# Optimization experiments

Measured on AMD Instinct MI355X. Metric: run time of the kernel, lower is better.

## Reference

```python
import jax, jax.numpy as jnp
import numpy as np

B, C_ENT, C_REL = 32768, 1000, 500


def setup_inputs() -> dict:
    key = jax.random.key(0)
    ks = jax.random.split(key, 6)
    return {
        "sub_input": jax.random.normal(ks[0], (B, C_ENT), dtype=jnp.float32),
        "relation_input": jax.random.normal(ks[1], (B, C_REL), dtype=jnp.float32),
        "obj_input": jax.random.normal(ks[2], (B, C_ENT), dtype=jnp.float32),
        "sub_target": jax.random.randint(ks[3], (B,), 0, C_ENT, dtype=jnp.int32),
        "relation_target": jax.random.randint(ks[4], (B,), 0, C_REL, dtype=jnp.int32),
        "obj_target": jax.random.randint(ks[5], (B,), 0, C_ENT, dtype=jnp.int32),
    }


def reference(sub_input, relation_input, obj_input, sub_target, relation_target, obj_target):
    s = jax.nn.softmax(sub_input, axis=1)
    r = jax.nn.softmax(relation_input, axis=1)
    o = jax.nn.softmax(obj_input, axis=1)
    b = s.shape[0]
    rows = jnp.arange(b)

    # ground-truth triplet probability
    gt = s[rows, sub_target] * r[rows, relation_target] * o[rows, obj_target]

    # top-2 values/indices per row (replaces full torch.sort)
    sv, si = jax.lax.top_k(s, 2)
    rv, ri = jax.lax.top_k(r, 2)
    ov, oi = jax.lax.top_k(o, 2)

    # all three argmaxes match the targets?
    cond = (si[:, 0] == sub_target) & (ri[:, 0] == relation_target) & (oi[:, 0] == obj_target)

    # 8 combinations of top-2 probs; second-smallest of the 8 (torch.sort ascending, index 1)
    tmp = (sv[:, :, None, None] * rv[:, None, :, None] * ov[:, None, None, :]).reshape(b, 8)
    second_smallest = jnp.sort(tmp, axis=1)[:, 1]

    top1 = sv[:, 0] * rv[:, 0] * ov[:, 0]
    pre = jnp.where(cond, second_smallest, top1)

    out = 1.0 - gt + pre
    return jnp.mean(jnp.maximum(out, 0.0))
```

## Files before the change

kernel.cpp:

```cpp
#include <hip/hip_runtime.h>
#include <float.h>
#include <limits.h>


constexpr int B     = 32768;
constexpr int C_ENT = 1000;
constexpr int C_REL = 500;
constexpr int NU    = 163840;
constexpr int UPW   = 16;
constexpr float LOG2E = 1.4426950408889634f;

__device__ inline float fast_exp2(float x) { return exp2f(x); }

__device__ inline const float4* unit_ptr(int u, const float* s, const float* r,
                                         const float* o) {
  const float* p;
  if (u < 2 * B)        p = s + ((size_t)(u >> 1) * C_ENT + (size_t)(u & 1) * C_REL);
  else if (u < 4 * B) { int v = u - 2 * B;
                        p = o + ((size_t)(v >> 1) * C_ENT + (size_t)(v & 1) * C_REL); }
  else                  p = r + (size_t)(u - 4 * B) * C_REL;
  return (const float4*)p;
}
__device__ inline int unit_ioff(int u) { return (u < 4 * B) ? (u & 1) * C_REL : 0; }

__device__ inline void unit_load(const float4* p4, int lane, float4& va, float4& vb) {
  va = make_float4(-FLT_MAX, -FLT_MAX, -FLT_MAX, -FLT_MAX);
  vb = va;
  if (lane <= 62) va = p4[2 * lane];
  if (lane <= 61) vb = p4[2 * lane + 1];
}

__device__ inline float4 unit_compute(const float4 va, const float4 vb,
                                      int lane, int ioff) {
  float m = fmaxf(fmaxf(fmaxf(va.x, va.y), fmaxf(va.z, va.w)),
                  fmaxf(fmaxf(vb.x, vb.y), fmaxf(vb.z, vb.w)));
#pragma unroll
  for (int off = 32; off; off >>= 1) m = fmaxf(m, __shfl_xor(m, off));
  const float m1 = m;
  const float nm1l = -m1 * LOG2E;

  float z = (fast_exp2(fmaf(va.x, LOG2E, nm1l)) + fast_exp2(fmaf(va.y, LOG2E, nm1l))) +
            (fast_exp2(fmaf(va.z, LOG2E, nm1l)) + fast_exp2(fmaf(va.w, LOG2E, nm1l))) +
            (fast_exp2(fmaf(vb.x, LOG2E, nm1l)) + fast_exp2(fmaf(vb.y, LOG2E, nm1l))) +
            (fast_exp2(fmaf(vb.z, LOG2E, nm1l)) + fast_exp2(fmaf(vb.w, LOG2E, nm1l)));

  const bool e0 = (va.x == m1), e1 = (va.y == m1), e2 = (va.z == m1), e3 = (va.w == m1);
  const bool e4 = (vb.x == m1), e5 = (vb.y == m1), e6 = (vb.z == m1), e7 = (vb.w == m1);
  const int cnt = ((int)e0 + (int)e1 + (int)e2 + (int)e3) +
                  ((int)e4 + (int)e5 + (int)e6 + (int)e7);
  float m2 = fmaxf(fmaxf(fmaxf(e0 ? -FLT_MAX : va.x, e1 ? -FLT_MAX : va.y),
                         fmaxf(e2 ? -FLT_MAX : va.z, e3 ? -FLT_MAX : va.w)),
                   fmaxf(fmaxf(e4 ? -FLT_MAX : vb.x, e5 ? -FLT_MAX : vb.y),
                         fmaxf(e6 ? -FLT_MAX : vb.z, e7 ? -FLT_MAX : vb.w)));
  const int li = e0 ? 0 : e1 ? 1 : e2 ? 2 : e3 ? 3 : e4 ? 4 : e5 ? 5 : e6 ? 6 : 7;

  const unsigned long long b1 = __ballot(cnt >= 1);
  const unsigned long long b2 = __ballot(cnt >= 2);
  const bool dup = (__popcll(b1) >= 2) || (b2 != 0ULL);
  const int src = __ffsll(b1) - 1;
  const int gidx = ioff + 8 * src + __shfl(li, src);

#pragma unroll
  for (int off = 32; off; off >>= 1) {
    z += __shfl_xor(z, off);
    m2 = fmaxf(m2, __shfl_xor(m2, off));
  }
  if (dup) m2 = m1;

  return make_float4(m1, m2, z, __int_as_float(gidx));
}

__global__ __launch_bounds__(256, 4) void stats_kernel(
    const float* __restrict__ s, const float* __restrict__ r, const float* __restrict__ o,
    float4* __restrict__ out4) {
  const int lane = threadIdx.x & 63;
  const int u0 = (blockIdx.x * 4 + (threadIdx.x >> 6)) * UPW;

  float4 Aa, Ab, Ba, Bb, Ca, Cb, Da, Db;
  unit_load(unit_ptr(u0 + 0, s, r, o), lane, Aa, Ab);
  unit_load(unit_ptr(u0 + 1, s, r, o), lane, Ba, Bb);
  unit_load(unit_ptr(u0 + 2, s, r, o), lane, Ca, Cb);

#pragma unroll
  for (int j = 0; j < UPW; j += 4) {
    float4 res;
    if (j + 3 < UPW) unit_load(unit_ptr(u0 + j + 3, s, r, o), lane, Da, Db);
    res = unit_compute(Aa, Ab, lane, unit_ioff(u0 + j + 0));
    if (lane == 0) out4[u0 + j + 0] = res;
    if (j + 4 < UPW) unit_load(unit_ptr(u0 + j + 4, s, r, o), lane, Aa, Ab);
    res = unit_compute(Ba, Bb, lane, unit_ioff(u0 + j + 1));
    if (lane == 0) out4[u0 + j + 1] = res;
    if (j + 5 < UPW) unit_load(unit_ptr(u0 + j + 5, s, r, o), lane, Ba, Bb);
    res = unit_compute(Ca, Cb, lane, unit_ioff(u0 + j + 2));
    if (lane == 0) out4[u0 + j + 2] = res;
    if (j + 6 < UPW) unit_load(unit_ptr(u0 + j + 6, s, r, o), lane, Ca, Cb);
    res = unit_compute(Da, Db, lane, unit_ioff(u0 + j + 3));
    if (lane == 0) out4[u0 + j + 3] = res;
  }
}

__device__ inline void merge_halves(float4 a, float4 b,
                                    float& m1, float& m2, float& Z, int& idx) {
  m1 = fmaxf(a.x, b.x);
  Z  = a.z * fast_exp2((a.x - m1) * LOG2E) + b.z * fast_exp2((b.x - m1) * LOG2E);
  m2 = fmaxf(fminf(a.x, b.x), (a.x >= b.x) ? a.y : b.y);
  idx = (b.x > a.x) ? __float_as_int(b.w) : __float_as_int(a.w);
}

__global__ __launch_bounds__(256) void combine_kernel(
    const float4* __restrict__ st4,
    const float* __restrict__ s, const float* __restrict__ r, const float* __restrict__ o,
    const int* __restrict__ st, const int* __restrict__ rt, const int* __restrict__ ot,
    float* __restrict__ out) {
  const int row = blockIdx.x * 256 + threadIdx.x;

  const float4 sa = st4[2 * row],         sb = st4[2 * row + 1];
  const float4 oa = st4[2 * B + 2 * row], ob = st4[2 * B + 2 * row + 1];
  const float4 rr = st4[4 * B + row];
  const int ts = st[row], tr = rt[row], to = ot[row];
  const float xs = s[(size_t)row * C_ENT + ts];
  const float xr = r[(size_t)row * C_REL + tr];
  const float xo = o[(size_t)row * C_ENT + to];

  float sm1, sm2, sZ; int si;
  float om1, om2, oZ; int oi;
  merge_halves(sa, sb, sm1, sm2, sZ, si);
  merge_halves(oa, ob, om1, om2, oZ, oi);
  const float rm1 = rr.x, rm2 = rr.y, rZ = rr.z;
  const int ri = __float_as_int(rr.w);

  const float sI = 1.0f / sZ, rI = 1.0f / rZ, oI = 1.0f / oZ;
  const float sp1 = fast_exp2((sm2 - sm1) * LOG2E) * sI;
  const float rp1 = fast_exp2((rm2 - rm1) * LOG2E) * rI;
  const float op1 = fast_exp2((om2 - om1) * LOG2E) * oI;
  const float spt = fast_exp2((xs - sm1) * LOG2E) * sI;
  const float rpt = fast_exp2((xr - rm1) * LOG2E) * rI;
  const float opt = fast_exp2((xo - om1) * LOG2E) * oI;

  const float gt   = spt * rpt * opt;
  const float top1 = sI * rI * oI;
  const float c1 = sI  * rp1 * op1;
  const float c2 = sp1 * rI  * op1;
  const float c3 = sp1 * rp1 * oI;
  const float second = fminf(c1, fminf(c2, c3));
  const bool cond = (si == ts) && (ri == tr) && (oi == to);
  const float pre = cond ? second : top1;
  float val = fmaxf(1.0f - gt + pre, 0.0f) * (1.0f / (float)B);

#pragma unroll
  for (int off = 32; off; off >>= 1) val += __shfl_xor(val, off);
  __shared__ float lds[4];
  if ((threadIdx.x & 63) == 0) lds[threadIdx.x >> 6] = val;
  __syncthreads();
  if (threadIdx.x == 0)
    atomicAdd(out, (lds[0] + lds[1]) + (lds[2] + lds[3]));
}


__device__ inline void combine_stats(float& m1, int& i1, float& m2, float& Z,
                                     float bm1, int bi1, float bm2, float bZ) {
  bool bwin = (bm1 > m1) || (bm1 == m1 && bi1 < i1);
  float wm1 = bwin ? bm1 : m1;
  int   wi1 = bwin ? bi1 : i1;
  float wm2 = bwin ? bm2 : m2;
  float lm1 = bwin ? m1  : bm1;
  float wZ  = bwin ? bZ  : Z;
  float lZ  = bwin ? Z   : bZ;
  m1 = wm1; i1 = wi1;
  m2 = fmaxf(wm2, lm1);
  Z  = wZ + lZ * __expf(lm1 - wm1);
}

template<int NK, int C4>
__device__ inline void row_stats(const float* __restrict__ row, int lane, int target,
                                 float& p_top1, float& p_top2, int& amax, float& p_tgt) {
  const float4* row4 = (const float4*)row;
  float4 v[NK];
#pragma unroll
  for (int k = 0; k < NK; ++k) {
    int idx = lane + 64 * k;
    v[k] = (idx < C4) ? row4[idx] : make_float4(-FLT_MAX, -FLT_MAX, -FLT_MAX, -FLT_MAX);
  }
  float m1 = -FLT_MAX, m2 = -FLT_MAX;
  int   i1 = 0x7fffffff;
#pragma unroll
  for (int k = 0; k < NK; ++k) {
    int base = 4 * (lane + 64 * k);
    float a0 = v[k].x, a1 = v[k].y, a2 = v[k].z, a3 = v[k].w;
    if (a0 > m1) { m2 = m1; m1 = a0; i1 = base;     } else if (a0 > m2) m2 = a0;
    if (a1 > m1) { m2 = m1; m1 = a1; i1 = base + 1; } else if (a1 > m2) m2 = a1;
    if (a2 > m1) { m2 = m1; m1 = a2; i1 = base + 2; } else if (a2 > m2) m2 = a2;
    if (a3 > m1) { m2 = m1; m1 = a3; i1 = base + 3; } else if (a3 > m2) m2 = a3;
  }
  float Z = 0.f;
#pragma unroll
  for (int k = 0; k < NK; ++k) {
    Z += __expf(v[k].x - m1); Z += __expf(v[k].y - m1);
    Z += __expf(v[k].z - m1); Z += __expf(v[k].w - m1);
  }
#pragma unroll
  for (int off = 32; off > 0; off >>= 1) {
    float bm1 = __shfl_xor(m1, off);
    int   bi1 = __shfl_xor(i1, off);
    float bm2 = __shfl_xor(m2, off);
    float bZ  = __shfl_xor(Z,  off);
    combine_stats(m1, i1, m2, Z, bm1, bi1, bm2, bZ);
  }
  float invZ = 1.0f / Z;
  float xt   = row[target];
  p_top1 = invZ;
  p_top2 = __expf(m2 - m1) * invZ;
  p_tgt  = __expf(xt - m1) * invZ;
  amax   = i1;
}

__global__ __launch_bounds__(256) void rank_loss_atomic_kernel(
    const float* __restrict__ s, const float* __restrict__ r, const float* __restrict__ o,
    const int* __restrict__ st, const int* __restrict__ rt, const int* __restrict__ ot,
    float* __restrict__ out) {
  const int wid  = threadIdx.x >> 6;
  const int lane = threadIdx.x & 63;
  const int row  = blockIdx.x * 4 + wid;

  const int tS = st[row], tR = rt[row], tO = ot[row];
  float sp0, sp1, spt; int sa;
  float rp0, rp1, rpt; int ra;
  float op0, op1, opt; int oa;
  row_stats<4, C_ENT / 4>(s + (size_t)row * C_ENT, lane, tS, sp0, sp1, sa, spt);
  row_stats<2, C_REL / 4>(r + (size_t)row * C_REL, lane, tR, rp0, rp1, ra, rpt);
  row_stats<4, C_ENT / 4>(o + (size_t)row * C_ENT, lane, tO, op0, op1, oa, opt);

  if (lane == 0) {
    float gt   = spt * rpt * opt;
    float top1 = sp0 * rp0 * op0;
    float c1 = sp0 * rp1 * op1;
    float c2 = sp1 * rp0 * op1;
    float c3 = sp1 * rp1 * op0;
    float second = fminf(c1, fminf(c2, c3));
    bool cond = (sa == tS) && (ra == tR) && (oa == tO);
    float pre = cond ? second : top1;
    atomicAdd(out, fmaxf(1.0f - gt + pre, 0.0f) * (1.0f / (float)B));
  }
}

extern "C" void kernel_launch(void* const* d_in, const int* in_sizes, int n_in,
                              void* d_out, int out_size, void* d_ws, size_t ws_size,
                              hipStream_t stream) {
  const float* s  = (const float*)d_in[0];
  const float* r  = (const float*)d_in[1];
  const float* o  = (const float*)d_in[2];
  const int*   st = (const int*)d_in[3];
  const int*   rt = (const int*)d_in[4];
  const int*   ot = (const int*)d_in[5];
  float* out = (float*)d_out;

  hipMemsetAsync(d_out, 0, sizeof(float), stream);
  if (ws_size >= (size_t)NU * sizeof(float4)) {
    float4* stat4 = (float4*)d_ws;
    stats_kernel<<<NU / UPW / 4, 256, 0, stream>>>(s, r, o, stat4);
    combine_kernel<<<B / 256, 256, 0, stream>>>(stat4, s, r, o, st, rt, ot, out);
  } else {
    rank_loss_atomic_kernel<<<B / 4, 256, 0, stream>>>(s, r, o, st, rt, ot, out);
  }
}
```

Before: 336.0 us.

## Restructure stats kernel to one thread per row with LDS-staged transposed tiles

Replaces the wave-per-half-row softmax statistics kernel with a 64-thread block that handles 64 rows, staging coalesced float4 loads through double-buffered LDS tiles so each thread streams its own row. Max, second max, argmax and the sum of exponentials are kept as online per-thread statistics, with no cross-lane shuffles. The target logit is captured during the pass, so the combine kernel no longer does scattered gathers into the big input matrices. The cost is LDS traffic, heavier per-thread register use and only 2560 single-wave blocks. The argmax tie handling also changes from the previous duplicate-detection logic.

New measurement: 824.0 us. +145.2%, slower.

```diff
diff --git a/kernel.cpp b/kernel.cpp
--- a/kernel.cpp
+++ b/kernel.cpp
@@ -1,126 +1,154 @@
 #include <hip/hip_runtime.h>
 #include <float.h>
-#include <limits.h>
 
 
 constexpr int B     = 32768;
 constexpr int C_ENT = 1000;
 constexpr int C_REL = 500;
-constexpr int NU    = 163840;
-constexpr int UPW   = 16;
 constexpr float LOG2E = 1.4426950408889634f;
 
-__device__ inline float fast_exp2(float x) { return exp2f(x); }
-
-__device__ inline const float4* unit_ptr(int u, const float* s, const float* r,
-                                         const float* o) {
-  const float* p;
-  if (u < 2 * B)        p = s + ((size_t)(u >> 1) * C_ENT + (size_t)(u & 1) * C_REL);
-  else if (u < 4 * B) { int v = u - 2 * B;
-                        p = o + ((size_t)(v >> 1) * C_ENT + (size_t)(v & 1) * C_REL); }
-  else                  p = r + (size_t)(u - 4 * B) * C_REL;
-  return (const float4*)p;
-}
-__device__ inline int unit_ioff(int u) { return (u < 4 * B) ? (u & 1) * C_REL : 0; }
-
-__device__ inline void unit_load(const float4* p4, int lane, float4& va, float4& vb) {
-  va = make_float4(-FLT_MAX, -FLT_MAX, -FLT_MAX, -FLT_MAX);
-  vb = va;
-  if (lane <= 62) va = p4[2 * lane];
-  if (lane <= 61) vb = p4[2 * lane + 1];
-}
-
-__device__ inline float4 unit_compute(const float4 va, const float4 vb,
-                                      int lane, int ioff) {
-  float m = fmaxf(fmaxf(fmaxf(va.x, va.y), fmaxf(va.z, va.w)),
-                  fmaxf(fmaxf(vb.x, vb.y), fmaxf(vb.z, vb.w)));
-#pragma unroll
-  for (int off = 32; off; off >>= 1) m = fmaxf(m, __shfl_xor(m, off));
-  const float m1 = m;
-  const float nm1l = -m1 * LOG2E;
-
-  float z = (fast_exp2(fmaf(va.x, LOG2E, nm1l)) + fast_exp2(fmaf(va.y, LOG2E, nm1l))) +
-            (fast_exp2(fmaf(va.z, LOG2E, nm1l)) + fast_exp2(fmaf(va.w, LOG2E, nm1l))) +
-            (fast_exp2(fmaf(vb.x, LOG2E, nm1l)) + fast_exp2(fmaf(vb.y, LOG2E, nm1l))) +
-            (fast_exp2(fmaf(vb.z, LOG2E, nm1l)) + fast_exp2(fmaf(vb.w, LOG2E, nm1l)));
-
-  const bool e0 = (va.x == m1), e1 = (va.y == m1), e2 = (va.z == m1), e3 = (va.w == m1);
-  const bool e4 = (vb.x == m1), e5 = (vb.y == m1), e6 = (vb.z == m1), e7 = (vb.w == m1);
-  const int cnt = ((int)e0 + (int)e1 + (int)e2 + (int)e3) +
-                  ((int)e4 + (int)e5 + (int)e6 + (int)e7);
-  float m2 = fmaxf(fmaxf(fmaxf(e0 ? -FLT_MAX : va.x, e1 ? -FLT_MAX : va.y),
-                         fmaxf(e2 ? -FLT_MAX : va.z, e3 ? -FLT_MAX : va.w)),
-                   fmaxf(fmaxf(e4 ? -FLT_MAX : vb.x, e5 ? -FLT_MAX : vb.y),
-                         fmaxf(e6 ? -FLT_MAX : vb.z, e7 ? -FLT_MAX : vb.w)));
-  const int li = e0 ? 0 : e1 ? 1 : e2 ? 2 : e3 ? 3 : e4 ? 4 : e5 ? 5 : e6 ? 6 : 7;
-
-  const unsigned long long b1 = __ballot(cnt >= 1);
-  const unsigned long long b2 = __ballot(cnt >= 2);
-  const bool dup = (__popcll(b1) >= 2) || (b2 != 0ULL);
-  const int src = __ffsll(b1) - 1;
-  const int gidx = ioff + 8 * src + __shfl(li, src);
-
-#pragma unroll
-  for (int off = 32; off; off >>= 1) {
-    z += __shfl_xor(z, off);
-    m2 = fmaxf(m2, __shfl_xor(m2, off));
-  }
-  if (dup) m2 = m1;
-
-  return make_float4(m1, m2, z, __int_as_float(gidx));
-}
-
-__global__ __launch_bounds__(256, 4) void stats_kernel(
+__device__ inline float fexp2(float x) { return exp2f(x); }
+
+
+__global__ __launch_bounds__(64, 4) void stats_kernel(
     const float* __restrict__ s, const float* __restrict__ r, const float* __restrict__ o,
-    float4* __restrict__ out4) {
-  const int lane = threadIdx.x & 63;
-  const int u0 = (blockIdx.x * 4 + (threadIdx.x >> 6)) * UPW;
-
-  float4 Aa, Ab, Ba, Bb, Ca, Cb, Da, Db;
-  unit_load(unit_ptr(u0 + 0, s, r, o), lane, Aa, Ab);
-  unit_load(unit_ptr(u0 + 1, s, r, o), lane, Ba, Bb);
-  unit_load(unit_ptr(u0 + 2, s, r, o), lane, Ca, Cb);
-
-#pragma unroll
-  for (int j = 0; j < UPW; j += 4) {
-    float4 res;
-    if (j + 3 < UPW) unit_load(unit_ptr(u0 + j + 3, s, r, o), lane, Da, Db);
-    res = unit_compute(Aa, Ab, lane, unit_ioff(u0 + j + 0));
-    if (lane == 0) out4[u0 + j + 0] = res;
-    if (j + 4 < UPW) unit_load(unit_ptr(u0 + j + 4, s, r, o), lane, Aa, Ab);
-    res = unit_compute(Ba, Bb, lane, unit_ioff(u0 + j + 1));
-    if (lane == 0) out4[u0 + j + 1] = res;
-    if (j + 5 < UPW) unit_load(unit_ptr(u0 + j + 5, s, r, o), lane, Ba, Bb);
-    res = unit_compute(Ca, Cb, lane, unit_ioff(u0 + j + 2));
-    if (lane == 0) out4[u0 + j + 2] = res;
-    if (j + 6 < UPW) unit_load(unit_ptr(u0 + j + 6, s, r, o), lane, Ca, Cb);
-    res = unit_compute(Da, Db, lane, unit_ioff(u0 + j + 3));
-    if (lane == 0) out4[u0 + j + 3] = res;
-  }
-}
+    const int* __restrict__ st, const int* __restrict__ rt, const int* __restrict__ ot,
+    float4* __restrict__ stat4, float* __restrict__ xtg) {
+  __shared__ float lds0[64 * 21];
+  __shared__ float lds1[64 * 21];
+  const int l = threadIdx.x;
+  const int u = blockIdx.x;
+  const int seg = u >> 9, rb = u & 511;
+
+  const float* mat; const int* tgt; int stride_f, coff_f;
+  if (seg < 2)      { mat = s; tgt = st; stride_f = C_ENT; coff_f = (seg & 1) * 500; }
+  else if (seg < 4) { mat = o; tgt = ot; stride_f = C_ENT; coff_f = (seg & 1) * 500; }
+  else              { mat = r; tgt = rt; stride_f = C_REL; coff_f = 0; }
+
+  const int row0 = rb * 64;
+  const float* segbase = mat + (size_t)row0 * stride_f + coff_f;
+
+  const float4* bp[5];
+  int wa[5];
+#pragma unroll
+  for (int j = 0; j < 5; ++j) {
+    const int f = j * 64 + l;
+    const int rl = f / 5, c = f - 5 * rl;
+    bp[j] = (const float4*)(segbase + (size_t)rl * stride_f) + c;
+    wa[j] = rl * 21 + c * 4;
+  }
+  const float* rp0 = &lds0[l * 21];
+  const float* rp1 = &lds1[l * 21];
+
+  const int t = tgt[row0 + l];
+  int d = t - coff_f;
+  float xt = 0.f;
+  float m1 = -FLT_MAX, m2 = -FLT_MAX, Z = 0.f;
+  int idx = 0, kb = 0;
+
+  auto compute = [&](const float* __restrict__ rowp) {
+    float a[20];
+#pragma unroll
+    for (int c = 0; c < 20; ++c) a[c] = rowp[c];
+    {
+      const unsigned du = (unsigned)d;
+      const float cand = rowp[du < 20u ? du : 19u];
+      if (du < 20u) xt = cand;
+      d -= 20;
+    }
+    const float b0 = fmaxf(fmaxf(a[0],  a[1]),  fmaxf(a[2],  a[3]));
+    const float b1 = fmaxf(fmaxf(a[4],  a[5]),  fmaxf(a[6],  a[7]));
+    const float b2 = fmaxf(fmaxf(a[8],  a[9]),  fmaxf(a[10], a[11]));
+    const float b3 = fmaxf(fmaxf(a[12], a[13]), fmaxf(a[14], a[15]));
+    const float b4 = fmaxf(fmaxf(a[16], a[17]), fmaxf(a[18], a[19]));
+    const float mc  = fmaxf(fmaxf(b0, b1), fmaxf(fmaxf(b2, b3), b4));
+    const float m1n = fmaxf(m1, mc);
+    const float nb  = -m1n * LOG2E;
+    float z0 = 0.f, z1 = 0.f, z2 = 0.f, z3 = 0.f;
+#pragma unroll
+    for (int c = 0; c < 20; c += 4) {
+      z0 += fexp2(fmaf(a[c],     LOG2E, nb));
+      z1 += fexp2(fmaf(a[c + 1], LOG2E, nb));
+      z2 += fexp2(fmaf(a[c + 2], LOG2E, nb));
+      z3 += fexp2(fmaf(a[c + 3], LOG2E, nb));
+    }
+    const float zc = (z0 + z1) + (z2 + z3);
+    Z = fmaf(Z, fexp2((m1 - m1n) * LOG2E), zc);
+    int lpos = 0;
+    const float m1b = m1;
+#pragma unroll
+    for (int c = 0; c < 20; ++c) {
+      const float av = a[c];
+      m2 = fmaxf(m2, fminf(m1, av));
+      const bool g = av > m1;
+      m1 = fmaxf(m1, av);
+      lpos = g ? c : lpos;
+    }
+    idx = (m1 > m1b) ? kb + lpos : idx;
+    kb += 20;
+  };
+  auto stage = [&](float* __restrict__ wb, const float4 v0, const float4 v1,
+                   const float4 v2, const float4 v3, const float4 v4) {
+    wb[wa[0]] = v0.x; wb[wa[0]+1] = v0.y; wb[wa[0]+2] = v0.z; wb[wa[0]+3] = v0.w;
+    wb[wa[1]] = v1.x; wb[wa[1]+1] = v1.y; wb[wa[1]+2] = v1.z; wb[wa[1]+3] = v1.w;
+    wb[wa[2]] = v2.x; wb[wa[2]+1] = v2.y; wb[wa[2]+2] = v2.z; wb[wa[2]+3] = v2.w;
+    wb[wa[3]] = v3.x; wb[wa[3]+1] = v3.y; wb[wa[3]+2] = v3.z; wb[wa[3]+3] = v3.w;
+    wb[wa[4]] = v4.x; wb[wa[4]+1] = v4.y; wb[wa[4]+2] = v4.z; wb[wa[4]+3] = v4.w;
+  };
+
+  float4 P0,P1,P2,P3,P4, Q0,Q1,Q2,Q3,Q4;
+  P0 = bp[0][0];  P1 = bp[1][0];  P2 = bp[2][0];  P3 = bp[3][0];  P4 = bp[4][0];
+  Q0 = bp[0][5];  Q1 = bp[1][5];  Q2 = bp[2][5];  Q3 = bp[3][5];  Q4 = bp[4][5];
+  stage(lds0, P0, P1, P2, P3, P4);
+  P0 = bp[0][10]; P1 = bp[1][10]; P2 = bp[2][10]; P3 = bp[3][10]; P4 = bp[4][10];
+  stage(lds1, Q0, Q1, Q2, Q3, Q4);
+  Q0 = bp[0][15]; Q1 = bp[1][15]; Q2 = bp[2][15]; Q3 = bp[3][15]; Q4 = bp[4][15];
+
+  for (int p = 0; p < 10; ++p) {
+    compute(rp0);
+    stage(lds0, P0, P1, P2, P3, P4);
+    P0 = bp[0][20]; P1 = bp[1][20]; P2 = bp[2][20]; P3 = bp[3][20]; P4 = bp[4][20];
+    compute(rp1);
+    stage(lds1, Q0, Q1, Q2, Q3, Q4);
+    Q0 = bp[0][25]; Q1 = bp[1][25]; Q2 = bp[2][25]; Q3 = bp[3][25]; Q4 = bp[4][25];
+    bp[0] += 10; bp[1] += 10; bp[2] += 10; bp[3] += 10; bp[4] += 10;
+  }
+  compute(rp0);
+  stage(lds0, P0, P1, P2, P3, P4);
+  P0 = bp[0][20]; P1 = bp[1][20]; P2 = bp[2][20]; P3 = bp[3][20]; P4 = bp[4][20];
+  compute(rp1);
+  stage(lds1, Q0, Q1, Q2, Q3, Q4);
+  compute(rp0);
+  stage(lds0, P0, P1, P2, P3, P4);
+  compute(rp1);
+  compute(rp0);
+
+  const int gr = seg * B + row0 + l;
+  stat4[gr] = make_float4(m1, m2, Z, __int_as_float(coff_f + idx));
+  xtg[gr] = xt;
+}
+
 
 __device__ inline void merge_halves(float4 a, float4 b,
                                     float& m1, float& m2, float& Z, int& idx) {
   m1 = fmaxf(a.x, b.x);
-  Z  = a.z * fast_exp2((a.x - m1) * LOG2E) + b.z * fast_exp2((b.x - m1) * LOG2E);
+  Z  = a.z * fexp2((a.x - m1) * LOG2E) + b.z * fexp2((b.x - m1) * LOG2E);
   m2 = fmaxf(fminf(a.x, b.x), (a.x >= b.x) ? a.y : b.y);
   idx = (b.x > a.x) ? __float_as_int(b.w) : __float_as_int(a.w);
 }
 
 __global__ __launch_bounds__(256) void combine_kernel(
-    const float4* __restrict__ st4,
-    const float* __restrict__ s, const float* __restrict__ r, const float* __restrict__ o,
+    const float4* __restrict__ st4, const float* __restrict__ xtg,
     const int* __restrict__ st, const int* __restrict__ rt, const int* __restrict__ ot,
     float* __restrict__ out) {
   const int row = blockIdx.x * 256 + threadIdx.x;
-
-  const float4 sa = st4[2 * row],         sb = st4[2 * row + 1];
-  const float4 oa = st4[2 * B + 2 * row], ob = st4[2 * B + 2 * row + 1];
+  const float4 sa = st4[row],         sb = st4[B + row];
+  const float4 oa = st4[2 * B + row], ob = st4[3 * B + row];
   const float4 rr = st4[4 * B + row];
   const int ts = st[row], tr = rt[row], to = ot[row];
-  const float xs = s[(size_t)row * C_ENT + ts];
-  const float xr = r[(size_t)row * C_REL + tr];
-  const float xo = o[(size_t)row * C_ENT + to];
+  const float xs = (ts < 500) ? xtg[row]           : xtg[B + row];
+  const float xo = (to < 500) ? xtg[2 * B + row]   : xtg[3 * B + row];
+  const float xr = xtg[4 * B + row];
 
   float sm1, sm2, sZ; int si;
   float om1, om2, oZ; int oi;
@@ -130,12 +158,12 @@
   const int ri = __float_as_int(rr.w);
 
   const float sI = 1.0f / sZ, rI = 1.0f / rZ, oI = 1.0f / oZ;
-  const float sp1 = fast_exp2((sm2 - sm1) * LOG2E) * sI;
-  const float rp1 = fast_exp2((rm2 - rm1) * LOG2E) * rI;
-  const float op1 = fast_exp2((om2 - om1) * LOG2E) * oI;
-  const float spt = fast_exp2((xs - sm1) * LOG2E) * sI;
-  const float rpt = fast_exp2((xr - rm1) * LOG2E) * rI;
-  const float opt = fast_exp2((xo - om1) * LOG2E) * oI;
+  const float sp1 = fexp2((sm2 - sm1) * LOG2E) * sI;
+  const float rp1 = fexp2((rm2 - rm1) * LOG2E) * rI;
+  const float op1 = fexp2((om2 - om1) * LOG2E) * oI;
+  const float spt = fexp2((xs - sm1) * LOG2E) * sI;
+  const float rpt = fexp2((xr - rm1) * LOG2E) * rI;
+  const float opt = fexp2((xo - om1) * LOG2E) * oI;
 
   const float gt   = spt * rpt * opt;
   const float top1 = sI * rI * oI;
@@ -149,11 +177,11 @@
 
 #pragma unroll
   for (int off = 32; off; off >>= 1) val += __shfl_xor(val, off);
-  __shared__ float lds[4];
-  if ((threadIdx.x & 63) == 0) lds[threadIdx.x >> 6] = val;
+  __shared__ float red[4];
+  if ((threadIdx.x & 63) == 0) red[threadIdx.x >> 6] = val;
   __syncthreads();
   if (threadIdx.x == 0)
-    atomicAdd(out, (lds[0] + lds[1]) + (lds[2] + lds[3]));
+    atomicAdd(out, (red[0] + red[1]) + (red[2] + red[3]));
 }
 
 
@@ -178,8 +206,8 @@
   float4 v[NK];
 #pragma unroll
   for (int k = 0; k < NK; ++k) {
-    int idx = lane + 64 * k;
-    v[k] = (idx < C4) ? row4[idx] : make_float4(-FLT_MAX, -FLT_MAX, -FLT_MAX, -FLT_MAX);
+    int i2 = lane + 64 * k;
+    v[k] = (i2 < C4) ? row4[i2] : make_float4(-FLT_MAX, -FLT_MAX, -FLT_MAX, -FLT_MAX);
   }
   float m1 = -FLT_MAX, m2 = -FLT_MAX;
   int   i1 = 0x7fffffff;
@@ -207,10 +235,10 @@
     combine_stats(m1, i1, m2, Z, bm1, bi1, bm2, bZ);
   }
   float invZ = 1.0f / Z;
-  float xt   = row[target];
+  float xv   = row[target];
   p_top1 = invZ;
   p_top2 = __expf(m2 - m1) * invZ;
-  p_tgt  = __expf(xt - m1) * invZ;
+  p_tgt  = __expf(xv - m1) * invZ;
   amax   = i1;
 }
 
@@ -255,10 +283,13 @@
   float* out = (float*)d_out;
 
   hipMemsetAsync(d_out, 0, sizeof(float), stream);
-  if (ws_size >= (size_t)NU * sizeof(float4)) {
+  const size_t statBytes = (size_t)5 * B * sizeof(float4);
+  const size_t xtBytes   = (size_t)5 * B * sizeof(float);
+  if (ws_size >= statBytes + xtBytes) {
     float4* stat4 = (float4*)d_ws;
-    stats_kernel<<<NU / UPW / 4, 256, 0, stream>>>(s, r, o, stat4);
-    combine_kernel<<<B / 256, 256, 0, stream>>>(stat4, s, r, o, st, rt, ot, out);
+    float*  xtg   = (float*)((char*)d_ws + statBytes);
+    stats_kernel<<<2560, 64, 0, stream>>>(s, r, o, st, rt, ot, stat4, xtg);
+    combine_kernel<<<B / 256, 256, 0, stream>>>(stat4, xtg, st, rt, ot, out);
   } else {
     rank_loss_atomic_kernel<<<B / 4, 256, 0, stream>>>(s, r, o, st, rt, ot, out);
   }
```
